# Kernel optimization log

Measured on AMD Instinct MI355X. Metric: run time of the kernel, lower is better.

The kernel has to match this reference:

```python
import jax, jax.numpy as jnp
import numpy as np

B, S, D = 4, 2048, 1024  # batch, seq_len, input_dim (= dk = dv)


def setup_inputs() -> dict:
    key = jax.random.key(0)
    kx, kq, kk, kv = jax.random.split(key, 4)
    scale = 1.0 / np.sqrt(D)
    return {
        "x": jax.random.normal(kx, (B, S, D), dtype=jnp.float32),
        "Wq": jax.random.normal(kq, (D, D), dtype=jnp.float32) * scale,
        "Wk": jax.random.normal(kk, (D, D), dtype=jnp.float32) * scale,
        "Wv": jax.random.normal(kv, (D, D), dtype=jnp.float32) * scale,
    }


def reference(x, Wq, Wk, Wv):
    # Linear projections (bias=False). W is [in, out].
    Q = jnp.einsum("bsd,de->bse", x, Wq)
    K = jnp.einsum("bsd,de->bse", x, Wk)
    V = jnp.einsum("bsd,de->bse", x, Wv)
    dk = Q.shape[-1]
    # scores: [B, S, S]
    scores = jnp.einsum("bqe,bke->bqk", Q, K) / jnp.sqrt(jnp.float32(dk))
    # causal mask: upper triangle (j > i) masked to -inf
    S_len = x.shape[1]
    causal = jnp.triu(jnp.ones((S_len, S_len), dtype=bool), k=1)
    scores = jnp.where(causal[None, :, :], -jnp.inf, scores)
    attn = jax.nn.softmax(scores, axis=-1)
    # dropout p=0.0 (eval): identity
    return jnp.einsum("bqk,bke->bqe", attn, V)
```

## Files before the change

### kernel.cpp

```cpp
#include <hip/hip_runtime.h>

#define S_LEN 2048
#define DMODEL 1024
#define NBATCH 4

typedef unsigned short u16;
typedef __bf16 bf16x8 __attribute__((ext_vector_type(8)));
typedef float f32x4 __attribute__((ext_vector_type(4)));

typedef __attribute__((address_space(3))) unsigned lds_u32;
typedef const __attribute__((address_space(1))) unsigned glb_u32;

__device__ __forceinline__ u16 f2bf(float f) {
  union { float f; unsigned u; } v;
  v.f = f;
  unsigned r = v.u + 0x7fffu + ((v.u >> 16) & 1u);
  return (u16)(r >> 16);
}

__device__ __forceinline__ float bf2f(u16 h) {
  union { unsigned u; float f; } v;
  v.u = ((unsigned)h) << 16;
  return v.f;
}

__global__ void convert_x_kernel(const float* __restrict__ x, u16* __restrict__ xb, long n) {
  long i = ((long)blockIdx.x * blockDim.x + threadIdx.x) * 4;
  long stride = (long)gridDim.x * blockDim.x * 4;
  for (; i < n; i += stride) {
    float4 v = *reinterpret_cast<const float4*>(x + i);
    ushort4 o;
    o.x = f2bf(v.x); o.y = f2bf(v.y); o.z = f2bf(v.z); o.w = f2bf(v.w);
    *reinterpret_cast<ushort4*>(xb + i) = o;
  }
}

__global__ void transpose_w_kernel(const float* __restrict__ W, u16* __restrict__ Wt) {
  __shared__ float tile[32][33];
  int tx = threadIdx.x, ty = threadIdx.y;
  int k0 = blockIdx.x * 32, n0 = blockIdx.y * 32;
#pragma unroll
  for (int i = 0; i < 32; i += 8)
    tile[ty + i][tx] = W[(long)(k0 + ty + i) * DMODEL + n0 + tx];
  __syncthreads();
#pragma unroll
  for (int i = 0; i < 32; i += 8)
    Wt[(long)(n0 + ty + i) * DMODEL + k0 + tx] = f2bf(tile[tx][ty + i]);
}


#define STG(SRCP, LD, ISB, H, T, BUFB) do { \
    const u16* _s = (SRCP) + (long)(H) * 128 * (LD) + (T) * 64; \
    char* _d = lds + (BUFB) * 65536 + ((ISB) ? 32768 : 0) + ((H) * 8 + w) * 2048; \
    __builtin_amdgcn_global_load_lds((glb_u32*)_s, (lds_u32*)_d, 16, 0, 0); \
    __builtin_amdgcn_global_load_lds((glb_u32*)(_s + 32), (lds_u32*)(_d + 1024), 16, 0, 0); \
  } while (0)

#define READ_A(QM) do { \
    _Pragma("unroll") \
    for (int _i = 0; _i < 4; ++_i) { \
      int _mp = (QM) * 8 + wm * 4 + _i; \
      af[_i][0] = *(const bf16x8*)(_Al + (_mp * 2 + 0) * 1024 + frag_off); \
      af[_i][1] = *(const bf16x8*)(_Al + (_mp * 2 + 1) * 1024 + frag_off); \
    } \
  } while (0)

#define READ_BQ(DST, QN) do { \
    _Pragma("unroll") \
    for (int _j = 0; _j < 2; ++_j) { \
      int _np = (QN) * 8 + wn * 2 + _j; \
      DST[_j][0] = *(const bf16x8*)(_Bl + (_np * 2 + 0) * 1024 + frag_off); \
      DST[_j][1] = *(const bf16x8*)(_Bl + (_np * 2 + 1) * 1024 + frag_off); \
    } \
  } while (0)

#define MFMA16(QM, QN, BREG) do { \
    _Pragma("unroll") \
    for (int _i = 0; _i < 4; ++_i) \
      _Pragma("unroll") \
      for (int _j = 0; _j < 2; ++_j) { \
        acc[QM][QN][_i][_j] = __builtin_amdgcn_mfma_f32_16x16x32_bf16(af[_i][0], BREG[_j][0], acc[QM][QN][_i][_j], 0, 0, 0); \
        acc[QM][QN][_i][_j] = __builtin_amdgcn_mfma_f32_16x16x32_bf16(af[_i][1], BREG[_j][1], acc[QM][QN][_i][_j], 0, 0, 0); \
      } \
  } while (0)

template<int CMODE, int CAUSAL>
__global__ __launch_bounds__(512, 2) void gemm256(
    const u16* __restrict__ A, const u16* __restrict__ B, void* __restrict__ Cptr,
    int lda, int ldb, int ldc, int Kdim,
    long sAz, long sBz, long sCz)
{
  int bm = blockIdx.x, bn = blockIdx.y, bz = blockIdx.z;
  if (CAUSAL == 1 && bn > bm) return;
  int Keff = Kdim;
  if (CAUSAL == 2) { int lim = (bm + 1) * 256; if (lim < Keff) Keff = lim; }
  int NT = Keff >> 6;

  const u16* Ab = A + (long)bz * sAz + (long)bm * 256 * lda;
  const u16* Bb = B + (long)bz * sBz + (long)bn * 256 * ldb;

  __shared__ char lds[131072];

  int tid = threadIdx.x;
  int lane = tid & 63, w = tid >> 6;
  int wm = w >> 2, wn = w & 3;
  int l15 = lane & 15, lhi = lane >> 4;
  int frag_off = (l15 * 64 + lhi * 16) ^ (((lane >> 3) & 1) << 5);

  int le = lane ^ ((lane >> 5) << 1);
  int lr = le >> 2;
  int kb = (le & 3) * 8;

  const u16* Asrc = Ab + (long)(w * 16 + lr) * lda + kb;
  const u16* Bsrc = Bb + (long)(w * 16 + lr) * ldb + kb;

  f32x4 acc[2][2][4][2];
#pragma unroll
  for (int a = 0; a < 2; ++a)
#pragma unroll
    for (int b = 0; b < 2; ++b)
#pragma unroll
      for (int c = 0; c < 4; ++c)
#pragma unroll
        for (int d = 0; d < 2; ++d)
          acc[a][b][c][d] = (f32x4){0.f, 0.f, 0.f, 0.f};

  STG(Asrc, lda, 0, 0, 0, 0); STG(Bsrc, ldb, 1, 0, 0, 0);
  STG(Asrc, lda, 0, 1, 0, 0); STG(Bsrc, ldb, 1, 1, 0, 0);
  STG(Asrc, lda, 0, 0, 1, 1); STG(Bsrc, ldb, 1, 0, 1, 1);
  asm volatile("s_waitcnt vmcnt(4)" ::: "memory");
  __builtin_amdgcn_s_barrier();

  for (int g = 0; g < NT; ++g) {
    int buf = g & 1;
    int t1 = g + 1; if (t1 >= NT) t1 -= NT;
    int t2 = g + 2; if (t2 >= NT) t2 -= NT;
    const char* _Al = lds + buf * 65536;
    const char* _Bl = _Al + 32768;
    bf16x8 af[4][2], b0[2][2], b1[2][2];

    READ_A(0);
    READ_BQ(b0, 0);
    STG(Asrc, lda, 0, 1, t1, buf ^ 1);
    __builtin_amdgcn_s_barrier();
    asm volatile("s_waitcnt lgkmcnt(0)" ::: "memory");
    __builtin_amdgcn_sched_barrier(0);
    __builtin_amdgcn_s_setprio(1);
    MFMA16(0, 0, b0);
    __builtin_amdgcn_s_setprio(0);
    __builtin_amdgcn_s_barrier();

    READ_BQ(b1, 1);
    STG(Bsrc, ldb, 1, 1, t1, buf ^ 1);
    __builtin_amdgcn_s_barrier();
    asm volatile("s_waitcnt lgkmcnt(0)" ::: "memory");
    __builtin_amdgcn_sched_barrier(0);
    __builtin_amdgcn_s_setprio(1);
    MFMA16(0, 1, b1);
    __builtin_amdgcn_s_setprio(0);
    __builtin_amdgcn_s_barrier();

    READ_A(1);
    STG(Asrc, lda, 0, 0, t2, buf);
    __builtin_amdgcn_s_barrier();
    asm volatile("s_waitcnt lgkmcnt(0)" ::: "memory");
    __builtin_amdgcn_sched_barrier(0);
    __builtin_amdgcn_s_setprio(1);
    MFMA16(1, 1, b1);
    __builtin_amdgcn_s_setprio(0);
    __builtin_amdgcn_s_barrier();

    STG(Bsrc, ldb, 1, 0, t2, buf);
    __builtin_amdgcn_s_barrier();
    __builtin_amdgcn_s_setprio(1);
    MFMA16(1, 0, b0);
    __builtin_amdgcn_s_setprio(0);
    asm volatile("s_waitcnt vmcnt(4)" ::: "memory");
    __builtin_amdgcn_s_barrier();
  }

  int Mbase = bm * 256, Nbase = bn * 256;
#pragma unroll
  for (int qm = 0; qm < 2; ++qm)
#pragma unroll
    for (int qn = 0; qn < 2; ++qn)
#pragma unroll
      for (int i = 0; i < 4; ++i)
#pragma unroll
        for (int j = 0; j < 2; ++j) {
          int r0 = Mbase + qm * 128 + wm * 64 + i * 16 + lhi * 4;
          int col = Nbase + qn * 128 + wn * 32 + j * 16 + l15;
          f32x4 v = acc[qm][qn][i][j];
          if constexpr (CMODE == 0) {
            float* C = (float*)Cptr + (long)bz * sCz;
#pragma unroll
            for (int r = 0; r < 4; ++r)
              C[(long)(r0 + r) * ldc + col] = v[r];
          } else if constexpr (CMODE == 1) {
            u16* C = (u16*)Cptr + (long)bz * sCz;
#pragma unroll
            for (int r = 0; r < 4; ++r)
              C[(long)(r0 + r) * ldc + col] = f2bf(v[r]);
          } else {
            if (col < 2048) {
              u16* dst = (u16*)Cptr + (col >= 1024 ? 8388608 : 0);
              int c = col & 1023;
#pragma unroll
              for (int r = 0; r < 4; ++r)
                dst[(long)(r0 + r) * 1024 + c] = f2bf(v[r]);
            } else {
              u16* Vt = (u16*)Cptr + 16777216;
              int e = col - 2048;
              int bb = r0 >> 11, s = r0 & 2047;
              ushort4 u;
              u.x = f2bf(v[0]); u.y = f2bf(v[1]); u.z = f2bf(v[2]); u.w = f2bf(v[3]);
              *reinterpret_cast<ushort4*>(Vt + ((long)bb * 1024 + e) * 2048 + s) = u;
            }
          }
        }
}

__global__ __launch_bounds__(256) void softmax1p(const u16* __restrict__ sc,
                                                 u16* __restrict__ P) {
  int q = blockIdx.x, b = blockIdx.y;
  const u16* srow = sc + ((long)b * S_LEN + q) * S_LEN;
  u16* prow = P + ((long)b * S_LEN + q) * S_LEN;
  int n = q + 1;
  int nz = ((q >> 8) + 1) << 8;
  int tid = threadIdx.x;
  int j0 = tid * 8;
  const float scale = 0.03125f;

  __shared__ float red[8];

  float vs[8];
#pragma unroll
  for (int e = 0; e < 8; ++e) vs[e] = -1e30f;
  if (j0 < n) {
    ushort4 a = *reinterpret_cast<const ushort4*>(srow + j0);
    ushort4 c = *reinterpret_cast<const ushort4*>(srow + j0 + 4);
    vs[0] = bf2f(a.x) * scale; vs[1] = bf2f(a.y) * scale;
    vs[2] = bf2f(a.z) * scale; vs[3] = bf2f(a.w) * scale;
    vs[4] = bf2f(c.x) * scale; vs[5] = bf2f(c.y) * scale;
    vs[6] = bf2f(c.z) * scale; vs[7] = bf2f(c.w) * scale;
#pragma unroll
    for (int e = 0; e < 8; ++e)
      if (j0 + e >= n) vs[e] = -1e30f;
  }

  float m = -1e30f;
#pragma unroll
  for (int e = 0; e < 8; ++e) m = fmaxf(m, vs[e]);
#pragma unroll
  for (int off = 32; off > 0; off >>= 1) m = fmaxf(m, __shfl_xor(m, off, 64));
  if ((tid & 63) == 0) red[tid >> 6] = m;
  __syncthreads();
  float ms = fmaxf(fmaxf(red[0], red[1]), fmaxf(red[2], red[3]));

  float p[8];
  float s = 0.f;
#pragma unroll
  for (int e = 0; e < 8; ++e) { p[e] = __expf(vs[e] - ms); s += (j0 + e < n) ? p[e] : 0.f; }
#pragma unroll
  for (int off = 32; off > 0; off >>= 1) s += __shfl_xor(s, off, 64);
  __syncthreads();
  if ((tid & 63) == 0) red[4 + (tid >> 6)] = s;
  __syncthreads();
  float inv = 1.f / (red[4] + red[5] + red[6] + red[7]);

  if (j0 < nz) {
    ushort4 o0, o1;
    o0.x = (j0 + 0 < n) ? f2bf(p[0] * inv) : (u16)0;
    o0.y = (j0 + 1 < n) ? f2bf(p[1] * inv) : (u16)0;
    o0.z = (j0 + 2 < n) ? f2bf(p[2] * inv) : (u16)0;
    o0.w = (j0 + 3 < n) ? f2bf(p[3] * inv) : (u16)0;
    o1.x = (j0 + 4 < n) ? f2bf(p[4] * inv) : (u16)0;
    o1.y = (j0 + 5 < n) ? f2bf(p[5] * inv) : (u16)0;
    o1.z = (j0 + 6 < n) ? f2bf(p[6] * inv) : (u16)0;
    o1.w = (j0 + 7 < n) ? f2bf(p[7] * inv) : (u16)0;
    *reinterpret_cast<ushort4*>(prow + j0) = o0;
    *reinterpret_cast<ushort4*>(prow + j0 + 4) = o1;
  }
}

extern "C" void kernel_launch(void* const* d_in, const int* in_sizes, int n_in,
                              void* d_out, int out_size, void* d_ws, size_t ws_size,
                              hipStream_t stream) {
  const float* x  = (const float*)d_in[0];
  const float* Wq = (const float*)d_in[1];
  const float* Wk = (const float*)d_in[2];
  const float* Wv = (const float*)d_in[3];
  float* out = (float*)d_out;

  char* ws = (char*)d_ws;
  u16* xb  = (u16*)(ws);
  u16* wtb = (u16*)(ws + 16777216);
  u16* Qb  = (u16*)(ws + 23068672);
  u16* Kb  = (u16*)(ws + 39845888);
  u16* Vtb = (u16*)(ws + 56623104);
  u16* scb = (u16*)(ws + 73400320);
  u16* P   = (u16*)(ws + 106954752);

  long nx = (long)NBATCH * S_LEN * DMODEL;
  convert_x_kernel<<<2048, 256, 0, stream>>>(x, xb, nx);

  dim3 tb(32, 8);
  transpose_w_kernel<<<dim3(32, 32), tb, 0, stream>>>(Wq, wtb);
  transpose_w_kernel<<<dim3(32, 32), tb, 0, stream>>>(Wk, wtb + 1024 * 1024);
  transpose_w_kernel<<<dim3(32, 32), tb, 0, stream>>>(Wv, wtb + 2 * 1024 * 1024);

  gemm256<3, 0><<<dim3(32, 12, 1), 512, 0, stream>>>(
      xb, wtb, Qb, DMODEL, DMODEL, 0, DMODEL, 0, 0, 0);

  gemm256<1, 1><<<dim3(8, 8, 4), 512, 0, stream>>>(
      Qb, Kb, scb, DMODEL, DMODEL, S_LEN, DMODEL,
      (long)S_LEN * DMODEL, (long)S_LEN * DMODEL, (long)S_LEN * S_LEN);

  softmax1p<<<dim3(S_LEN, NBATCH), 256, 0, stream>>>(scb, P);

  gemm256<0, 2><<<dim3(8, 4, 4), 512, 0, stream>>>(
      P, Vtb, out, S_LEN, S_LEN, DMODEL, S_LEN,
      (long)S_LEN * S_LEN, (long)DMODEL * S_LEN, (long)S_LEN * DMODEL);
}
```

Measured before the change: 185.7 us.

## Add 128x256 tiled GEMM kernel for QKV projection and PV product

Adds a gemm128 kernel with a 128x256 output tile and 96KB of double-buffered LDS, launch bounds allowing two blocks per CU, and B-tile loads split into two halves so they interleave with the MFMA phases. The fused QKV projection and the causal P·V GEMM now use it, with twice as many blocks in M. This targets poor CU fill: the old 256x256 tiles gave 384 and 128 blocks, and the causal PV grid was also unevenly loaded. The cost is less reuse per block and more global traffic for the B operand.

```diff
diff --git a/kernel.cpp b/kernel.cpp
--- a/kernel.cpp
+++ b/kernel.cpp
@@ -47,7 +47,6 @@
   for (int i = 0; i < 32; i += 8)
     Wt[(long)(n0 + ty + i) * DMODEL + k0 + tx] = f2bf(tile[tx][ty + i]);
 }
-
 
 #define STG(SRCP, LD, ISB, H, T, BUFB) do { \
     const u16* _s = (SRCP) + (long)(H) * 128 * (LD) + (T) * 64; \
@@ -201,23 +200,155 @@
 #pragma unroll
             for (int r = 0; r < 4; ++r)
               C[(long)(r0 + r) * ldc + col] = f2bf(v[r]);
-          } else {
-            if (col < 2048) {
-              u16* dst = (u16*)Cptr + (col >= 1024 ? 8388608 : 0);
-              int c = col & 1023;
-#pragma unroll
-              for (int r = 0; r < 4; ++r)
-                dst[(long)(r0 + r) * 1024 + c] = f2bf(v[r]);
-            } else {
-              u16* Vt = (u16*)Cptr + 16777216;
-              int e = col - 2048;
-              int bb = r0 >> 11, s = r0 & 2047;
-              ushort4 u;
-              u.x = f2bf(v[0]); u.y = f2bf(v[1]); u.z = f2bf(v[2]); u.w = f2bf(v[3]);
-              *reinterpret_cast<ushort4*>(Vt + ((long)bb * 1024 + e) * 2048 + s) = u;
-            }
           }
         }
+}
+
+template<int CMODE, int CAUSAL>
+__global__ __launch_bounds__(512, 2) void gemm128(
+    const u16* __restrict__ A, const u16* __restrict__ B, void* __restrict__ Cptr,
+    int lda, int ldb, int ldc, int Kdim,
+    long sAz, long sBz, long sCz)
+{
+  int bm = blockIdx.x, bn = blockIdx.y, bz = blockIdx.z;
+  int Keff = Kdim;
+  if (CAUSAL == 2) { int lim = (bm + 1) * 128; if (lim < Keff) Keff = lim; }
+  int NT = Keff >> 6;
+
+  const u16* Ab = A + (long)bz * sAz + (long)bm * 128 * lda;
+  const u16* Bb = B + (long)bz * sBz + (long)bn * 256 * ldb;
+
+  __shared__ char lds[98304];
+
+  int tid = threadIdx.x;
+  int lane = tid & 63, w = tid >> 6;
+  int wm = w >> 2, wn = w & 3;
+  int l15 = lane & 15, lhi = lane >> 4;
+  int frag_off = (l15 * 64 + lhi * 16) ^ (((lane >> 3) & 1) << 5);
+
+  int le = lane ^ ((lane >> 5) << 1);
+  int lr = le >> 2;
+  int kb = (le & 3) * 8;
+
+  const u16* Asrc = Ab + (long)(w * 16 + lr) * lda + kb;
+  const u16* Bsrc = Bb + (long)(w * 16 + lr) * ldb + kb;
+
+#define STG_A1(T, BUFB) do { \
+    const u16* _s = Asrc + (T) * 64; \
+    char* _d = lds + (BUFB) * 49152 + w * 2048; \
+    __builtin_amdgcn_global_load_lds((glb_u32*)_s, (lds_u32*)_d, 16, 0, 0); \
+    __builtin_amdgcn_global_load_lds((glb_u32*)(_s + 32), (lds_u32*)(_d + 1024), 16, 0, 0); \
+  } while (0)
+#define STG_B1H0(T, BUFB) do { \
+    const u16* _s = Bsrc + (T) * 64; \
+    char* _d = lds + (BUFB) * 49152 + 16384 + w * 2048; \
+    __builtin_amdgcn_global_load_lds((glb_u32*)_s, (lds_u32*)_d, 16, 0, 0); \
+    __builtin_amdgcn_global_load_lds((glb_u32*)(_s + 32), (lds_u32*)(_d + 1024), 16, 0, 0); \
+  } while (0)
+#define STG_B1H1(T, BUFB) do { \
+    const u16* _s = Bsrc + (long)128 * ldb + (T) * 64; \
+    char* _d = lds + (BUFB) * 49152 + 16384 + (8 + w) * 2048; \
+    __builtin_amdgcn_global_load_lds((glb_u32*)_s, (lds_u32*)_d, 16, 0, 0); \
+    __builtin_amdgcn_global_load_lds((glb_u32*)(_s + 32), (lds_u32*)(_d + 1024), 16, 0, 0); \
+  } while (0)
+
+  f32x4 acc[4][4];
+#pragma unroll
+  for (int i = 0; i < 4; ++i)
+#pragma unroll
+    for (int j = 0; j < 4; ++j)
+      acc[i][j] = (f32x4){0.f, 0.f, 0.f, 0.f};
+
+  STG_A1(0, 0); STG_B1H0(0, 0); STG_B1H1(0, 0);
+  asm volatile("s_waitcnt vmcnt(0)" ::: "memory");
+  __builtin_amdgcn_s_barrier();
+
+  for (int g = 0; g < NT; ++g) {
+    int buf = g & 1;
+    const char* _Al = lds + buf * 49152;
+    const char* _Bl = _Al + 16384;
+    bf16x8 af[4][2], bfr[2][2];
+
+#pragma unroll
+    for (int i = 0; i < 4; ++i) {
+      af[i][0] = *(const bf16x8*)(_Al + ((wm * 4 + i) * 2 + 0) * 1024 + frag_off);
+      af[i][1] = *(const bf16x8*)(_Al + ((wm * 4 + i) * 2 + 1) * 1024 + frag_off);
+    }
+#pragma unroll
+    for (int j = 0; j < 2; ++j) {
+      bfr[j][0] = *(const bf16x8*)(_Bl + ((wn * 4 + j) * 2 + 0) * 1024 + frag_off);
+      bfr[j][1] = *(const bf16x8*)(_Bl + ((wn * 4 + j) * 2 + 1) * 1024 + frag_off);
+    }
+    if (g + 1 < NT) { STG_A1(g + 1, buf ^ 1); STG_B1H0(g + 1, buf ^ 1); }
+    __builtin_amdgcn_s_barrier();
+    asm volatile("s_waitcnt lgkmcnt(0)" ::: "memory");
+    __builtin_amdgcn_sched_barrier(0);
+    __builtin_amdgcn_s_setprio(1);
+#pragma unroll
+    for (int i = 0; i < 4; ++i)
+#pragma unroll
+      for (int j = 0; j < 2; ++j) {
+        acc[i][j] = __builtin_amdgcn_mfma_f32_16x16x32_bf16(af[i][0], bfr[j][0], acc[i][j], 0, 0, 0);
+        acc[i][j] = __builtin_amdgcn_mfma_f32_16x16x32_bf16(af[i][1], bfr[j][1], acc[i][j], 0, 0, 0);
+      }
+    __builtin_amdgcn_s_setprio(0);
+    __builtin_amdgcn_s_barrier();
+
+#pragma unroll
+    for (int j = 0; j < 2; ++j) {
+      bfr[j][0] = *(const bf16x8*)(_Bl + ((wn * 4 + 2 + j) * 2 + 0) * 1024 + frag_off);
+      bfr[j][1] = *(const bf16x8*)(_Bl + ((wn * 4 + 2 + j) * 2 + 1) * 1024 + frag_off);
+    }
+    if (g + 1 < NT) STG_B1H1(g + 1, buf ^ 1);
+    __builtin_amdgcn_s_barrier();
+    asm volatile("s_waitcnt lgkmcnt(0)" ::: "memory");
+    __builtin_amdgcn_sched_barrier(0);
+    __builtin_amdgcn_s_setprio(1);
+#pragma unroll
+    for (int i = 0; i < 4; ++i)
+#pragma unroll
+      for (int j = 0; j < 2; ++j) {
+        acc[i][2 + j] = __builtin_amdgcn_mfma_f32_16x16x32_bf16(af[i][0], bfr[j][0], acc[i][2 + j], 0, 0, 0);
+        acc[i][2 + j] = __builtin_amdgcn_mfma_f32_16x16x32_bf16(af[i][1], bfr[j][1], acc[i][2 + j], 0, 0, 0);
+      }
+    __builtin_amdgcn_s_setprio(0);
+    asm volatile("s_waitcnt vmcnt(0)" ::: "memory");
+    __builtin_amdgcn_s_barrier();
+  }
+#undef STG_A1
+#undef STG_B1H0
+#undef STG_B1H1
+
+  int Mbase = bm * 128, Nbase = bn * 256;
+#pragma unroll
+  for (int i = 0; i < 4; ++i)
+#pragma unroll
+    for (int j = 0; j < 4; ++j) {
+      int r0 = Mbase + wm * 64 + i * 16 + lhi * 4;
+      int col = Nbase + wn * 64 + j * 16 + l15;
+      f32x4 v = acc[i][j];
+      if constexpr (CMODE == 0) {
+        float* C = (float*)Cptr + (long)bz * sCz;
+#pragma unroll
+        for (int r = 0; r < 4; ++r)
+          C[(long)(r0 + r) * ldc + col] = v[r];
+      } else {
+        if (col < 2048) {
+          u16* dst = (u16*)Cptr + (col >= 1024 ? 8388608 : 0);
+          int c = col & 1023;
+#pragma unroll
+          for (int r = 0; r < 4; ++r)
+            dst[(long)(r0 + r) * 1024 + c] = f2bf(v[r]);
+        } else {
+          u16* Vt = (u16*)Cptr + 16777216;
+          int e = col - 2048;
+          int bb = r0 >> 11, s = r0 & 2047;
+          ushort4 u;
+          u.x = f2bf(v[0]); u.y = f2bf(v[1]); u.z = f2bf(v[2]); u.w = f2bf(v[3]);
+          *reinterpret_cast<ushort4*>(Vt + ((long)bb * 1024 + e) * 2048 + s) = u;
+        }
+      }
+    }
 }
 
 __global__ __launch_bounds__(256) void softmax1p(const u16* __restrict__ sc,
@@ -309,7 +440,7 @@
   transpose_w_kernel<<<dim3(32, 32), tb, 0, stream>>>(Wk, wtb + 1024 * 1024);
   transpose_w_kernel<<<dim3(32, 32), tb, 0, stream>>>(Wv, wtb + 2 * 1024 * 1024);
 
-  gemm256<3, 0><<<dim3(32, 12, 1), 512, 0, stream>>>(
+  gemm128<3, 0><<<dim3(64, 12, 1), 512, 0, stream>>>(
       xb, wtb, Qb, DMODEL, DMODEL, 0, DMODEL, 0, 0, 0);
 
   gemm256<1, 1><<<dim3(8, 8, 4), 512, 0, stream>>>(
@@ -318,7 +449,7 @@
 
   softmax1p<<<dim3(S_LEN, NBATCH), 256, 0, stream>>>(scb, P);
 
-  gemm256<0, 2><<<dim3(8, 4, 4), 512, 0, stream>>>(
+  gemm128<0, 2><<<dim3(16, 4, 4), 512, 0, stream>>>(
       P, Vtb, out, S_LEN, S_LEN, DMODEL, S_LEN,
       (long)S_LEN * S_LEN, (long)DMODEL * S_LEN, (long)S_LEN * DMODEL);
 }
```

Result: faster. 170.7 us (-8.1%).
